# Kernel optimization log

Hardware: AMD Instinct MI355X
Metric: run time of the kernel (lower is better)

The kernel has to match this reference:

```python
import jax, jax.numpy as jnp
import numpy as np

D_MODEL = 1024
NUM_HEAD = 16
HEAD_DIM = D_MODEL // NUM_HEAD
S, B = 2048, 2


def setup_inputs() -> dict:
    key = jax.random.key(0)
    ks = jax.random.split(key, 8)
    q = jax.random.normal(ks[0], (S, B, D_MODEL), dtype=jnp.float32)
    k = jax.random.normal(ks[1], (S, B, D_MODEL), dtype=jnp.float32)
    v = jax.random.normal(ks[2], (S, B, D_MODEL), dtype=jnp.float32)
    attn_mask = jnp.zeros((S, S), dtype=jnp.float32)
    # xavier_uniform_ bound for square (D,D) linear: sqrt(6/(D+D))
    bound = float(np.sqrt(6.0 / (D_MODEL + D_MODEL)))
    def w(k_):
        return jax.random.uniform(k_, (D_MODEL, D_MODEL), jnp.float32, -bound, bound)
    Wq, Wk, Wv, Wo = w(ks[3]), w(ks[4]), w(ks[5]), w(ks[6])
    zb = jnp.zeros((D_MODEL,), jnp.float32)
    return {"q": q, "k": k, "v": v, "attn_mask": attn_mask,
            "Wq": Wq, "bq": zb, "Wk": Wk, "bk": zb,
            "Wv": Wv, "bv": zb, "Wo": Wo, "bo": zb}


def reference(q, k, v, attn_mask, Wq, bq, Wk, bk, Wv, bv, Wo, bo):
    s, b, d = q.shape
    h, hd = NUM_HEAD, HEAD_DIM
    # QKV projections (torch Linear: x @ W.T + b)
    qp = q @ Wq.T + bq  # (S,B,D)
    kp = k @ Wk.T + bk
    vp = v @ Wv.T + bv
    # (S,B,H,Dh) -> permute(2,1,0,3) -> (H,B,S,Dh)
    qh = jnp.transpose(qp.reshape(s, b, h, hd), (2, 1, 0, 3))
    kh = jnp.transpose(kp.reshape(s, b, h, hd), (2, 1, 0, 3))
    vh = jnp.transpose(vp.reshape(s, b, h, hd), (2, 1, 0, 3))
    scores = jnp.einsum('hbqd,hbkd->hbqk', qh, kh) / jnp.sqrt(jnp.float32(hd))
    scores = scores + attn_mask  # additive mask broadcast over (H,B,*,*)
    weights = jax.nn.softmax(scores, axis=-1)
    out = jnp.einsum('hbqk,hbkd->hbqd', weights, vh)  # (H,B,S,Dh)
    # Faithful to original: raw contiguous view (H,B,S,Dh) -> (S,B,D)
    out = out.reshape(s, b, d)
    return out @ Wo.T + bo
```

## Files before the change

### kernel.cpp

```cpp
#include <hip/hip_runtime.h>
#include <hip/hip_bf16.h>
#include <cstdint>
#include <cstddef>

typedef unsigned short u16;
typedef short bf16x8 __attribute__((ext_vector_type(8)));
typedef short bf16x4 __attribute__((ext_vector_type(4)));
typedef unsigned short u16x8 __attribute__((ext_vector_type(8)));
typedef unsigned short u16x4 __attribute__((ext_vector_type(4)));
typedef float f32x4 __attribute__((ext_vector_type(4)));

#define S_LEN 2048
#define BATCH 2
#define DM 1024
#define NHEAD 16
#define HDIM 64
#define MROWS (S_LEN * BATCH)
#define LOG2E 1.44269504088896340736f
#define KSPLIT 2
#define SPAN (S_LEN / KSPLIT)
#define NROWS (NHEAD * BATCH * S_LEN)

__device__ __forceinline__ u16 f32_to_bf16(float f) {
  union { float f; uint32_t u; } v; v.f = f;
  uint32_t u = v.u;
  u += 0x7FFFu + ((u >> 16) & 1u);
  return (u16)(u >> 16);
}
__device__ __forceinline__ u16 cvt_bf16(float f) {
  __hip_bfloat16 h = __float2bfloat16(f);
  return *reinterpret_cast<u16*>(&h);
}
__device__ __forceinline__ float bf2f(u16 x) {
  union { float f; uint32_t u; } v; v.u = ((uint32_t)x) << 16; return v.f;
}

__device__ __forceinline__ void gload_lds16(const void* g, void* l) {
  __builtin_amdgcn_global_load_lds(
      (const __attribute__((address_space(1))) void*)g,
      (__attribute__((address_space(3))) void*)l, 16, 0, 0);
}

__device__ __forceinline__ bf16x4 tr_read(const void* lp) {
  bf16x4 d;
  auto p = (const __attribute__((address_space(3))) short*)lp;
  asm volatile("ds_read_b64_tr_b16 %0, %1" : "=v"(d) : "v"(p));
  return d;
}

#if __has_builtin(__builtin_amdgcn_mfma_f32_16x16x16_bf16)
#define MFMA16(a, b, c) __builtin_amdgcn_mfma_f32_16x16x16_bf16(a, b, c, 0, 0, 0)
#elif __has_builtin(__builtin_amdgcn_mfma_f32_16x16x16bf16_1k)
#define MFMA16(a, b, c) __builtin_amdgcn_mfma_f32_16x16x16bf16_1k(a, b, c, 0, 0, 0)
#else
__device__ __forceinline__ f32x4 mfma16_asm(bf16x4 a, bf16x4 b, f32x4 c) {
  f32x4 d;
  asm volatile("v_mfma_f32_16x16x16_bf16 %0, %1, %2, %3\n\ts_nop 7\n\ts_nop 7"
               : "=&v"(d) : "v"(a), "v"(b), "v"(c));
  return d;
}
#define MFMA16(a, b, c) mfma16_asm(a, b, c)
#endif

__global__ void cast4_f32_bf16(const float* __restrict__ s0, u16* __restrict__ d0,
                               const float* __restrict__ s1, u16* __restrict__ d1,
                               const float* __restrict__ s2, u16* __restrict__ d2,
                               const float* __restrict__ s3, u16* __restrict__ d3,
                               float4 scales, int n8) {
  const int which = blockIdx.y;
  const float* src = which == 0 ? s0 : which == 1 ? s1 : which == 2 ? s2 : s3;
  u16* dst = which == 0 ? d0 : which == 1 ? d1 : which == 2 ? d2 : d3;
  const float sc = which == 0 ? scales.x : which == 1 ? scales.y : which == 2 ? scales.z : scales.w;
  int i = blockIdx.x * blockDim.x + threadIdx.x;
  const int stride = gridDim.x * blockDim.x;
  for (; i < n8; i += stride) {
    const float4* s = (const float4*)(src + (size_t)i * 8);
    float4 a = s[0];
    float4 b = s[1];
    u16x8 o;
    o[0] = f32_to_bf16(a.x * sc); o[1] = f32_to_bf16(a.y * sc);
    o[2] = f32_to_bf16(a.z * sc); o[3] = f32_to_bf16(a.w * sc);
    o[4] = f32_to_bf16(b.x * sc); o[5] = f32_to_bf16(b.y * sc);
    o[6] = f32_to_bf16(b.z * sc); o[7] = f32_to_bf16(b.w * sc);
    *(u16x8*)(dst + (size_t)i * 8) = o;
  }
}

template <int MODE>
__device__ __forceinline__ void gemm_body(
    const u16* __restrict__ A, const u16* __restrict__ Bw, const float* __restrict__ bias,
    float* __restrict__ outF, u16* __restrict__ outP, float oscale,
    u16* As, u16* Bs)
{
  const int K = DM, N = DM;
  const int tid = threadIdx.x;
  const int wave = tid >> 6, lane = tid & 63;
  const int l15 = lane & 15, l4 = lane >> 4;
  const int wr = wave >> 1, wc = wave & 1;
  const int rowBase = blockIdx.y * 128, colBase = blockIdx.x * 64;

  f32x4 acc[4][2];
#pragma unroll
  for (int m = 0; m < 4; ++m)
#pragma unroll
    for (int n = 0; n < 2; ++n) acc[m][n] = (f32x4){0.f, 0.f, 0.f, 0.f};

  for (int k0 = 0; k0 < K; k0 += 32) {
#pragma unroll
    for (int c = 0; c < 2; ++c) {
      const int ldsbyte = wave * 2048 + c * 1024;
      const int elt = (ldsbyte >> 1) + lane * 8;
      const int r = elt >> 5, cc = elt & 31;
      gload_lds16(A + (size_t)(rowBase + r) * K + k0 + cc, (char*)As + ldsbyte);
    }
    {
      const int ldsbyte = wave * 1024;
      const int elt = (ldsbyte >> 1) + lane * 8;
      const int r = elt >> 5, cc = elt & 31;
      gload_lds16(Bw + (size_t)(colBase + r) * K + k0 + cc, (char*)Bs + ldsbyte);
    }
    __syncthreads();

    bf16x8 af[4], bfr[2];
#pragma unroll
    for (int m = 0; m < 4; ++m)
      af[m] = *(const bf16x8*)&As[(wr * 64 + m * 16 + l15) * 32 + 8 * l4];
#pragma unroll
    for (int n = 0; n < 2; ++n)
      bfr[n] = *(const bf16x8*)&Bs[(wc * 32 + n * 16 + l15) * 32 + 8 * l4];
#pragma unroll
    for (int m = 0; m < 4; ++m)
#pragma unroll
      for (int n = 0; n < 2; ++n)
        acc[m][n] = __builtin_amdgcn_mfma_f32_16x16x32_bf16(af[m], bfr[n], acc[m][n], 0, 0, 0);
    __syncthreads();
  }

#pragma unroll
  for (int m = 0; m < 4; ++m)
#pragma unroll
    for (int n = 0; n < 2; ++n)
#pragma unroll
      for (int j = 0; j < 4; ++j) {
        const int row = rowBase + wr * 64 + m * 16 + 4 * l4 + j;
        const int col = colBase + wc * 32 + n * 16 + l15;
        const float vv = (acc[m][n][j] + bias[col]) * oscale;
        if (MODE == 0) {
          const int s = row >> 1, b = row & 1, h = col >> 6, dh = col & 63;
          outP[((size_t)(h * BATCH + b) * S_LEN + s) * HDIM + dh] = f32_to_bf16(vv);
        } else {
          outF[(size_t)row * N + col] = vv;
        }
      }
}

__global__ __launch_bounds__(256) void gemm_qkv(
    const u16* __restrict__ Aq, const u16* __restrict__ Ak, const u16* __restrict__ Av,
    const u16* __restrict__ Wq, const u16* __restrict__ Wk, const u16* __restrict__ Wv,
    const float* __restrict__ bq, const float* __restrict__ bk, const float* __restrict__ bv,
    u16* __restrict__ Oq, u16* __restrict__ Ok, u16* __restrict__ Ov, float qscale)
{
  __shared__ u16 As[128 * 32];
  __shared__ u16 Bs[64 * 32];
  const int z = blockIdx.z;
  const u16* A  = z == 0 ? Aq : z == 1 ? Ak : Av;
  const u16* W  = z == 0 ? Wq : z == 1 ? Wk : Wv;
  const float* b = z == 0 ? bq : z == 1 ? bk : bv;
  u16* O = z == 0 ? Oq : z == 1 ? Ok : Ov;
  const float sc = z == 0 ? qscale : 1.f;
  gemm_body<0>(A, W, b, nullptr, O, sc, As, Bs);
}

__global__ __launch_bounds__(256) void gemm_out(
    const u16* __restrict__ A, const u16* __restrict__ W, const float* __restrict__ bias,
    float* __restrict__ outF)
{
  __shared__ u16 As[128 * 32];
  __shared__ u16 Bs[64 * 32];
  gemm_body<1>(A, W, bias, outF, nullptr, 1.f, As, Bs);
}

__device__ __forceinline__ void stageK_swz(const u16* __restrict__ Kp, int kt, u16* dst, int tid) {
#pragma unroll
  for (int h = 0; h < 2; ++h) {
    const int c = tid + 256 * h;
    const int r = c >> 3, x = c & 7;
    gload_lds16(Kp + (size_t)(kt + r) * HDIM + (x ^ (r & 7)) * 8, (char*)dst + 16 * c);
  }
}
__device__ __forceinline__ void stageV(const u16* __restrict__ Vp, int kt, u16* dst, int tid) {
#pragma unroll
  for (int h = 0; h < 2; ++h) {
    const int c = tid + 256 * h;
    const int key = 4 * ((c >> 3) & 15) + ((c >> 1) & 3);
    const int dh  = 16 * (c >> 7) + 8 * (c & 1);
    gload_lds16(Vp + (size_t)(kt + key) * HDIM + dh, (char*)dst + 16 * c);
  }
}

__global__ __launch_bounds__(256, 4) void flash_attn(
    const u16* __restrict__ Qh, const u16* __restrict__ Kh, const u16* __restrict__ Vh,
    const u16* __restrict__ maskb, u16* __restrict__ Opart, float2* __restrict__ mlp)
{
  const int hb = blockIdx.y;
  const int z  = blockIdx.z;
  const int qb = blockIdx.x * 128;
  const int kbase = z * SPAN;
  const u16* Qp = Qh + (size_t)hb * S_LEN * HDIM;
  const u16* Kp = Kh + (size_t)hb * S_LEN * HDIM + (size_t)kbase * HDIM;
  const u16* Vp = Vh + (size_t)hb * S_LEN * HDIM + (size_t)kbase * HDIM;
  const u16* mp = maskb + kbase;
  const int tid = threadIdx.x;
  const int wave = tid >> 6, lane = tid & 63;
  const int l15 = lane & 15, l4 = lane >> 4;
  const int qrow0 = qb + wave * 32 + l15;
  const int qrow1 = qrow0 + 16;

  __shared__ u16 Klds[2][4096];
  __shared__ u16 Vlds[2][4096];

  bf16x8 bq[2][2];
  bq[0][0] = *(const bf16x8*)&Qp[(size_t)qrow0 * HDIM + 8 * l4];
  bq[0][1] = *(const bf16x8*)&Qp[(size_t)qrow0 * HDIM + 32 + 8 * l4];
  bq[1][0] = *(const bf16x8*)&Qp[(size_t)qrow1 * HDIM + 8 * l4];
  bq[1][1] = *(const bf16x8*)&Qp[(size_t)qrow1 * HDIM + 32 + 8 * l4];

  stageK_swz(Kp, 0, &Klds[0][0], tid);
  stageV(Vp, 0, &Vlds[0][0], tid);

  float m_run[2] = {-1e30f, -1e30f}, l_run[2] = {0.f, 0.f};
  f32x4 oacc[2][4];
#pragma unroll
  for (int f = 0; f < 2; ++f)
#pragma unroll
    for (int D = 0; D < 4; ++D) oacc[f][D] = (f32x4){0.f, 0.f, 0.f, 0.f};

  __syncthreads();

  for (int kt = 0; kt < SPAN; kt += 64) {
    const int cur = (kt >> 6) & 1;
    if (kt + 64 < SPAN) {
      stageK_swz(Kp, kt + 64, &Klds[cur ^ 1][0], tid);
      stageV(Vp, kt + 64, &Vlds[cur ^ 1][0], tid);
    }
    u16x4 mc[2][4];
#pragma unroll
    for (int kb = 0; kb < 4; ++kb) {
      mc[0][kb] = *(const u16x4*)&mp[(size_t)qrow0 * S_LEN + kt + 16 * kb + 4 * l4];
      mc[1][kb] = *(const u16x4*)&mp[(size_t)qrow1 * S_LEN + kt + 16 * kb + 4 * l4];
    }

    bf16x4 pb[2][4];
#pragma unroll
    for (int f = 0; f < 2; ++f) {
      f32x4 st[4];
#pragma unroll
      for (int kb = 0; kb < 4; ++kb) {
        const int r = 16 * kb + l15;
        const int s0 = (l4 ^ (l15 & 7)) * 8;
        const int s1 = ((l4 + 4) ^ (l15 & 7)) * 8;
        bf16x8 k0 = *(const bf16x8*)&Klds[cur][r * 64 + s0];
        bf16x8 k1 = *(const bf16x8*)&Klds[cur][r * 64 + s1];
        f32x4 zz = (f32x4){0.f, 0.f, 0.f, 0.f};
        zz = __builtin_amdgcn_mfma_f32_16x16x32_bf16(k0, bq[f][0], zz, 0, 0, 0);
        zz = __builtin_amdgcn_mfma_f32_16x16x32_bf16(k1, bq[f][1], zz, 0, 0, 0);
        st[kb] = zz;
      }
      float p[16];
#pragma unroll
      for (int kb = 0; kb < 4; ++kb)
#pragma unroll
        for (int j = 0; j < 4; ++j)
          p[4 * kb + j] = st[kb][j] + bf2f((u16)mc[f][kb][j]);

      float t0 = fmaxf(fmaxf(p[0], p[1]), fmaxf(p[2], p[3]));
      float t1 = fmaxf(fmaxf(p[4], p[5]), fmaxf(p[6], p[7]));
      float t2 = fmaxf(fmaxf(p[8], p[9]), fmaxf(p[10], p[11]));
      float t3 = fmaxf(fmaxf(p[12], p[13]), fmaxf(p[14], p[15]));
      float tm = fmaxf(fmaxf(t0, t1), fmaxf(t2, t3));
      tm = fmaxf(tm, __shfl_xor(tm, 16));
      tm = fmaxf(tm, __shfl_xor(tm, 32));

      if (!__all(tm - m_run[f] <= 11.0f)) {
        const float mn_ = fmaxf(m_run[f], tm);
        const float fac = exp2f(m_run[f] - mn_);
#pragma unroll
        for (int D = 0; D < 4; ++D)
#pragma unroll
          for (int j = 0; j < 4; ++j) oacc[f][D][j] *= fac;
        l_run[f] *= fac;
        m_run[f] = mn_;
      }

      float rs = 0.f;
#pragma unroll
      for (int kb = 0; kb < 4; ++kb)
#pragma unroll
        for (int e = 0; e < 4; ++e) {
          const float pe = exp2f(p[4 * kb + e] - m_run[f]);
          rs += pe;
          pb[f][kb][e] = (short)cvt_bf16(pe);
        }
      rs += __shfl_xor(rs, 16);
      rs += __shfl_xor(rs, 32);
      l_run[f] += rs;
    }

    const char* vb = (const char*)&Vlds[cur][0] + 8 * lane;
#pragma unroll
    for (int g = 0; g < 2; ++g) {
      bf16x4 va[2][4];
#pragma unroll
      for (int D = 0; D < 2; ++D)
#pragma unroll
        for (int kb = 0; kb < 4; ++kb)
          va[D][kb] = tr_read(vb + 2048 * (2 * g + D) + 512 * kb);
      asm volatile("s_waitcnt lgkmcnt(0)" ::: "memory");
      __builtin_amdgcn_sched_barrier(0);
#pragma unroll
      for (int D = 0; D < 2; ++D)
#pragma unroll
        for (int kb = 0; kb < 4; ++kb) {
          oacc[0][2 * g + D] = MFMA16(va[D][kb], pb[0][kb], oacc[0][2 * g + D]);
          oacc[1][2 * g + D] = MFMA16(va[D][kb], pb[1][kb], oacc[1][2 * g + D]);
        }
    }

    __syncthreads();
  }

  u16* Oz = Opart + (size_t)z * NROWS * HDIM;
#pragma unroll
  for (int f = 0; f < 2; ++f) {
    const float inv = 1.0f / l_run[f];
    const int qr = f == 0 ? qrow0 : qrow1;
    const size_t row = (size_t)hb * S_LEN + qr;
#pragma unroll
    for (int D = 0; D < 4; ++D) {
      u16x4 ov;
#pragma unroll
      for (int j = 0; j < 4; ++j) ov[j] = f32_to_bf16(oacc[f][D][j] * inv);
      *(u16x4*)&Oz[row * HDIM + 16 * D + 4 * l4] = ov;
    }
    if (l4 == 0) mlp[(size_t)z * NROWS + row] = make_float2(m_run[f], l_run[f]);
  }
}

__global__ __launch_bounds__(256) void fa_combine(
    const u16* __restrict__ Opart, const float2* __restrict__ mlp, u16* __restrict__ Ob)
{
  const int idx = blockIdx.x * blockDim.x + threadIdx.x;
  const int row = idx >> 4, c = idx & 15;
  float2 ml[KSPLIT];
  float m = -1e30f;
#pragma unroll
  for (int zz = 0; zz < KSPLIT; ++zz) {
    ml[zz] = mlp[(size_t)zz * NROWS + row];
    m = fmaxf(m, ml[zz].x);
  }
  float w[KSPLIT], tot = 0.f;
#pragma unroll
  for (int zz = 0; zz < KSPLIT; ++zz) {
    w[zz] = exp2f(ml[zz].x - m) * ml[zz].y;
    tot += w[zz];
  }
  const float inv = 1.f / tot;
  const size_t off = (size_t)row * HDIM + 4 * c;
  float a0 = 0.f, a1 = 0.f, a2 = 0.f, a3 = 0.f;
#pragma unroll
  for (int zz = 0; zz < KSPLIT; ++zz) {
    const u16x4 o = *(const u16x4*)&Opart[(size_t)zz * NROWS * HDIM + off];
    const float wz = w[zz] * inv;
    a0 += wz * bf2f((u16)o[0]);
    a1 += wz * bf2f((u16)o[1]);
    a2 += wz * bf2f((u16)o[2]);
    a3 += wz * bf2f((u16)o[3]);
  }
  u16x4 o;
  o[0] = f32_to_bf16(a0); o[1] = f32_to_bf16(a1);
  o[2] = f32_to_bf16(a2); o[3] = f32_to_bf16(a3);
  *(u16x4*)&Ob[off] = o;
}

extern "C" void kernel_launch(void* const* d_in, const int* in_sizes, int n_in,
                              void* d_out, int out_size, void* d_ws, size_t ws_size,
                              hipStream_t stream) {
  const float* q    = (const float*)d_in[0];
  const float* k    = (const float*)d_in[1];
  const float* v    = (const float*)d_in[2];
  const float* mask = (const float*)d_in[3];
  const float* Wq   = (const float*)d_in[4];
  const float* bq   = (const float*)d_in[5];
  const float* Wk   = (const float*)d_in[6];
  const float* bk   = (const float*)d_in[7];
  const float* Wv   = (const float*)d_in[8];
  const float* bv   = (const float*)d_in[9];
  const float* Wo   = (const float*)d_in[10];
  const float* bo   = (const float*)d_in[11];
  float* out = (float*)d_out;

  char* ws = (char*)d_ws;
  const size_t MB = 1024 * 1024;
  u16*  Qh    = (u16*)(ws + 0 * MB);
  u16*  Kh    = (u16*)(ws + 8 * MB);
  u16*  Vh    = (u16*)(ws + 16 * MB);
  u16*  maskb = (u16*)(ws + 24 * MB);
  u16*  wob   = (u16*)(ws + 32 * MB);
  u16*  Ob    = (u16*)(ws + 34 * MB);
  u16*  qb_   = (u16*)(ws + 42 * MB);
  u16*  kb_   = (u16*)(ws + 50 * MB);
  u16*  vb_   = (u16*)(ws + 58 * MB);
  u16*  wqb   = (u16*)(ws + 66 * MB);
  u16*  wkb   = (u16*)(ws + 68 * MB);
  u16*  wvb   = (u16*)(ws + 70 * MB);
  u16*  Opart = (u16*)(ws + 42 * MB);
  float2* mlp = (float2*)(ws + 58 * MB);

  const int n8_t = MROWS * DM / 8;
  const int n8_w = DM * DM / 8;
  cast4_f32_bf16<<<dim3(1024, 4), 256, 0, stream>>>(
      q, qb_, k, kb_, v, vb_, mask, maskb,
      make_float4(1.f, 1.f, 1.f, LOG2E), n8_t);
  cast4_f32_bf16<<<dim3(256, 4), 256, 0, stream>>>(
      Wq, wqb, Wk, wkb, Wv, wvb, Wo, wob,
      make_float4(1.f, 1.f, 1.f, 1.f), n8_w);

  const float qscale = 0.125f * LOG2E;
  gemm_qkv<<<dim3(DM / 64, MROWS / 128, 3), 256, 0, stream>>>(
      qb_, kb_, vb_, wqb, wkb, wvb, bq, bk, bv, Qh, Kh, Vh, qscale);

  flash_attn<<<dim3(S_LEN / 128, NHEAD * BATCH, KSPLIT), 256, 0, stream>>>(
      Qh, Kh, Vh, maskb, Opart, mlp);
  fa_combine<<<NROWS * 16 / 256, 256, 0, stream>>>(Opart, mlp, Ob);

  gemm_out<<<dim3(DM / 64, MROWS / 128), 256, 0, stream>>>(Ob, wob, bo, out);
}
```

Measured before the change: 184.8 us.

## Use 128x128 tiles for QKV GEMM and compute softmax row sums via MFMA

The QKV projection GEMM moves from 128x64 to 128x128 output tiles, so each wave computes a 64x64 sub-tile with 16 MFMAs per k-step. This raises operand reuse from shared memory but halves the block count and raises register pressure. Separately, flash attention now accumulates the softmax denominator with an MFMA against a vector of ones, replacing the scalar sum and cross-lane shuffles. The row sum is therefore taken over bf16-rounded probabilities, which changes numerics slightly.

```diff
diff --git a/kernel.cpp b/kernel.cpp
--- a/kernel.cpp
+++ b/kernel.cpp
@@ -87,7 +87,70 @@
 }
 
 template <int MODE>
-__device__ __forceinline__ void gemm_body(
+__device__ __forceinline__ void gemm_body128(
+    const u16* __restrict__ A, const u16* __restrict__ Bw, const float* __restrict__ bias,
+    float* __restrict__ outF, u16* __restrict__ outP, float oscale,
+    u16* As, u16* Bs)
+{
+  const int K = DM, N = DM;
+  const int tid = threadIdx.x;
+  const int wave = tid >> 6, lane = tid & 63;
+  const int l15 = lane & 15, l4 = lane >> 4;
+  const int wr = wave >> 1, wc = wave & 1;
+  const int rowBase = blockIdx.y * 128, colBase = blockIdx.x * 128;
+
+  f32x4 acc[4][4];
+#pragma unroll
+  for (int m = 0; m < 4; ++m)
+#pragma unroll
+    for (int n = 0; n < 4; ++n) acc[m][n] = (f32x4){0.f, 0.f, 0.f, 0.f};
+
+  for (int k0 = 0; k0 < K; k0 += 32) {
+#pragma unroll
+    for (int c = 0; c < 2; ++c) {
+      const int ldsbyte = wave * 2048 + c * 1024;
+      const int elt = (ldsbyte >> 1) + lane * 8;
+      const int r = elt >> 5, cc = elt & 31;
+      gload_lds16(A + (size_t)(rowBase + r) * K + k0 + cc, (char*)As + ldsbyte);
+      gload_lds16(Bw + (size_t)(colBase + r) * K + k0 + cc, (char*)Bs + ldsbyte);
+    }
+    __syncthreads();
+
+    bf16x8 af[4], bfr[4];
+#pragma unroll
+    for (int m = 0; m < 4; ++m)
+      af[m] = *(const bf16x8*)&As[(wr * 64 + m * 16 + l15) * 32 + 8 * l4];
+#pragma unroll
+    for (int n = 0; n < 4; ++n)
+      bfr[n] = *(const bf16x8*)&Bs[(wc * 64 + n * 16 + l15) * 32 + 8 * l4];
+#pragma unroll
+    for (int m = 0; m < 4; ++m)
+#pragma unroll
+      for (int n = 0; n < 4; ++n)
+        acc[m][n] = __builtin_amdgcn_mfma_f32_16x16x32_bf16(af[m], bfr[n], acc[m][n], 0, 0, 0);
+    __syncthreads();
+  }
+
+#pragma unroll
+  for (int m = 0; m < 4; ++m)
+#pragma unroll
+    for (int n = 0; n < 4; ++n)
+#pragma unroll
+      for (int j = 0; j < 4; ++j) {
+        const int row = rowBase + wr * 64 + m * 16 + 4 * l4 + j;
+        const int col = colBase + wc * 64 + n * 16 + l15;
+        const float vv = (acc[m][n][j] + bias[col]) * oscale;
+        if (MODE == 0) {
+          const int s = row >> 1, b = row & 1, h = col >> 6, dh = col & 63;
+          outP[((size_t)(h * BATCH + b) * S_LEN + s) * HDIM + dh] = f32_to_bf16(vv);
+        } else {
+          outF[(size_t)row * N + col] = vv;
+        }
+      }
+}
+
+template <int MODE>
+__device__ __forceinline__ void gemm_body64(
     const u16* __restrict__ A, const u16* __restrict__ Bw, const float* __restrict__ bias,
     float* __restrict__ outF, u16* __restrict__ outP, float oscale,
     u16* As, u16* Bs)
@@ -161,14 +224,14 @@
     u16* __restrict__ Oq, u16* __restrict__ Ok, u16* __restrict__ Ov, float qscale)
 {
   __shared__ u16 As[128 * 32];
-  __shared__ u16 Bs[64 * 32];
+  __shared__ u16 Bs[128 * 32];
   const int z = blockIdx.z;
   const u16* A  = z == 0 ? Aq : z == 1 ? Ak : Av;
   const u16* W  = z == 0 ? Wq : z == 1 ? Wk : Wv;
   const float* b = z == 0 ? bq : z == 1 ? bk : bv;
   u16* O = z == 0 ? Oq : z == 1 ? Ok : Ov;
   const float sc = z == 0 ? qscale : 1.f;
-  gemm_body<0>(A, W, b, nullptr, O, sc, As, Bs);
+  gemm_body128<0>(A, W, b, nullptr, O, sc, As, Bs);
 }
 
 __global__ __launch_bounds__(256) void gemm_out(
@@ -177,7 +240,7 @@
 {
   __shared__ u16 As[128 * 32];
   __shared__ u16 Bs[64 * 32];
-  gemm_body<1>(A, W, bias, outF, nullptr, 1.f, As, Bs);
+  gemm_body64<1>(A, W, bias, outF, nullptr, 1.f, As, Bs);
 }
 
 __device__ __forceinline__ void stageK_swz(const u16* __restrict__ Kp, int kt, u16* dst, int tid) {
@@ -228,12 +291,20 @@
   stageK_swz(Kp, 0, &Klds[0][0], tid);
   stageV(Vp, 0, &Vlds[0][0], tid);
 
-  float m_run[2] = {-1e30f, -1e30f}, l_run[2] = {0.f, 0.f};
+  const u16 one_bf = 0x3F80;
+  bf16x4 ones;
+  ones[0] = (short)one_bf; ones[1] = (short)one_bf;
+  ones[2] = (short)one_bf; ones[3] = (short)one_bf;
+
+  float m_run[2] = {-1e30f, -1e30f};
+  f32x4 lacc[2];
   f32x4 oacc[2][4];
 #pragma unroll
-  for (int f = 0; f < 2; ++f)
+  for (int f = 0; f < 2; ++f) {
+    lacc[f] = (f32x4){0.f, 0.f, 0.f, 0.f};
 #pragma unroll
     for (int D = 0; D < 4; ++D) oacc[f][D] = (f32x4){0.f, 0.f, 0.f, 0.f};
+  }
 
   __syncthreads();
 
@@ -288,22 +359,20 @@
         for (int D = 0; D < 4; ++D)
 #pragma unroll
           for (int j = 0; j < 4; ++j) oacc[f][D][j] *= fac;
-        l_run[f] *= fac;
+#pragma unroll
+        for (int j = 0; j < 4; ++j) lacc[f][j] *= fac;
         m_run[f] = mn_;
       }
 
-      float rs = 0.f;
 #pragma unroll
       for (int kb = 0; kb < 4; ++kb)
 #pragma unroll
-        for (int e = 0; e < 4; ++e) {
-          const float pe = exp2f(p[4 * kb + e] - m_run[f]);
-          rs += pe;
-          pb[f][kb][e] = (short)cvt_bf16(pe);
-        }
-      rs += __shfl_xor(rs, 16);
-      rs += __shfl_xor(rs, 32);
-      l_run[f] += rs;
+        for (int e = 0; e < 4; ++e)
+          pb[f][kb][e] = (short)cvt_bf16(exp2f(p[4 * kb + e] - m_run[f]));
+
+#pragma unroll
+      for (int kb = 0; kb < 4; ++kb)
+        lacc[f] = MFMA16(ones, pb[f][kb], lacc[f]);
     }
 
     const char* vb = (const char*)&Vlds[cur][0] + 8 * lane;
@@ -332,7 +401,8 @@
   u16* Oz = Opart + (size_t)z * NROWS * HDIM;
 #pragma unroll
   for (int f = 0; f < 2; ++f) {
-    const float inv = 1.0f / l_run[f];
+    const float lr = lacc[f][0];
+    const float inv = 1.0f / lr;
     const int qr = f == 0 ? qrow0 : qrow1;
     const size_t row = (size_t)hb * S_LEN + qr;
 #pragma unroll
@@ -342,7 +412,7 @@
       for (int j = 0; j < 4; ++j) ov[j] = f32_to_bf16(oacc[f][D][j] * inv);
       *(u16x4*)&Oz[row * HDIM + 16 * D + 4 * l4] = ov;
     }
-    if (l4 == 0) mlp[(size_t)z * NROWS + row] = make_float2(m_run[f], l_run[f]);
+    if (l4 == 0) mlp[(size_t)z * NROWS + row] = make_float2(m_run[f], lr);
   }
 }
 
@@ -426,7 +496,7 @@
       make_float4(1.f, 1.f, 1.f, 1.f), n8_w);
 
   const float qscale = 0.125f * LOG2E;
-  gemm_qkv<<<dim3(DM / 64, MROWS / 128, 3), 256, 0, stream>>>(
+  gemm_qkv<<<dim3(DM / 128, MROWS / 128, 3), 256, 0, stream>>>(
       qb_, kb_, vb_, wqb, wkb, wvb, bq, bk, bv, Qh, Kh, Vh, qscale);
 
   flash_attn<<<dim3(S_LEN / 128, NHEAD * BATCH, KSPLIT), 256, 0, stream>>>(
```

After: 197.2 us. 6.7% more time.
